# Optimization experiments

Hardware: AMD Instinct MI355X
Metric: run time of the kernel (lower is better)

The kernel has to match this reference:

```python
import jax, jax.numpy as jnp
import numpy as np

B, L, D = 4096, 200, 256
NUM_ITEMS, NUM_DT = 200000, 64


def setup_inputs() -> dict:
    key = jax.random.key(0)
    k1, k2, k3, k4, k5, k6 = jax.random.split(key, 6)
    items_pad = jax.random.randint(k1, (B, L), 0, NUM_ITEMS)
    dts_pad = jax.random.randint(k2, (B, L), 0, NUM_DT)
    mask = jnp.ones((B, L), dtype=bool)
    pos_items = jax.random.randint(k3, (B,), 0, NUM_ITEMS)
    neg_items = jax.random.randint(k4, (B,), 0, NUM_ITEMS)
    # embedding tables; row 0 zeroed to emulate padding_idx=0
    item_emb = jax.random.normal(k5, (NUM_ITEMS, D), dtype=jnp.float32).at[0].set(0.0)
    dt_gate = jax.random.normal(k6, (NUM_DT, 1), dtype=jnp.float32).at[0].set(0.0)
    raw_tau = jnp.float32(0.0)
    return {"items_pad": items_pad, "dts_pad": dts_pad, "mask": mask,
            "pos_items": pos_items, "neg_items": neg_items,
            "item_emb": item_emb, "dt_gate": dt_gate, "raw_tau": raw_tau}


def reference(items_pad, dts_pad, mask, pos_items, neg_items, item_emb, dt_gate, raw_tau):
    tau = jax.nn.softplus(raw_tau) + 1e-6
    k = item_emb[items_pad]                       # [B,L,D] history item embeddings
    gate = dt_gate[dts_pad, 0]                    # [B,L]  time-gate scalars

    def cand_aware_uservec(cand_items):
        q = item_emb[cand_items]                  # [B,D]
        sim = jnp.einsum('bld,bd->bl', k, q)      # candidate-aware similarity
        logits = jnp.where(mask, sim * gate / tau, -jnp.inf)
        attn = jax.nn.softmax(logits, axis=1)     # [B,L]
        u = jnp.einsum('bl,bld->bd', attn, k)     # weighted sum (bmm)
        return u, attn, q

    u_pos, attn_pos, q_pos = cand_aware_uservec(pos_items)
    u_neg, _, q_neg = cand_aware_uservec(neg_items)
    pos_score = jnp.sum(u_pos * q_pos, axis=-1)   # [B]
    neg_score = jnp.sum(u_neg * q_neg, axis=-1)   # [B]
    return pos_score, neg_score, attn_pos
```

## Files before the change

### kernel.cpp

```cpp
#include <hip/hip_runtime.h>
#include <math.h>

#define B_ 4096
#define L_ 200
#define D_ 256

__device__ __forceinline__ void dot8(const float* __restrict__ kp,
                                     const float qp[8], const float qn[8],
                                     float& sp, float& sn) {
    const float4 k0 = *(const float4*)kp;
    const float4 k1 = *(const float4*)(kp + 4);
    float a = 0.f, c = 0.f;
    a = fmaf(k0.x, qp[0], a); c = fmaf(k0.x, qn[0], c);
    a = fmaf(k0.y, qp[1], a); c = fmaf(k0.y, qn[1], c);
    a = fmaf(k0.z, qp[2], a); c = fmaf(k0.z, qn[2], c);
    a = fmaf(k0.w, qp[3], a); c = fmaf(k0.w, qn[3], c);
    a = fmaf(k1.x, qp[4], a); c = fmaf(k1.x, qn[4], c);
    a = fmaf(k1.y, qp[5], a); c = fmaf(k1.y, qn[5], c);
    a = fmaf(k1.z, qp[6], a); c = fmaf(k1.z, qn[6], c);
    a = fmaf(k1.w, qp[7], a); c = fmaf(k1.w, qn[7], c);
    sp = a; sn = c;
}

__global__ __launch_bounds__(256) void sic_f32(
    const int* __restrict__ items, const int* __restrict__ dts,
    const int* __restrict__ pos_items, const int* __restrict__ neg_items,
    const float* __restrict__ emb, const float* __restrict__ dt_gate,
    const float* __restrict__ raw_tau, float* __restrict__ out)
{
    const int b    = blockIdx.x;
    const int tid  = threadIdx.x;
    const int lane = tid & 63;
    const int wave = tid >> 6;
    const int half = lane >> 5;
    const int hl   = lane & 31;

    __shared__ int   s_items[L_];
    __shared__ float s_gate[L_];
    __shared__ float s_simp[L_], s_simn[L_];
    __shared__ float s_red[16];

    if (tid < L_) {
        s_items[tid] = items[b * L_ + tid];
        s_gate[tid]  = dt_gate[dts[b * L_ + tid]];
    }

    float qp[8], qn[8];
    {
        const float* pq = emb + (size_t)pos_items[b] * D_ + (size_t)hl * 8;
        const float* nq = emb + (size_t)neg_items[b] * D_ + (size_t)hl * 8;
        const float4 a0 = *(const float4*)pq, a1 = *(const float4*)(pq + 4);
        const float4 c0 = *(const float4*)nq, c1 = *(const float4*)(nq + 4);
        qp[0]=a0.x; qp[1]=a0.y; qp[2]=a0.z; qp[3]=a0.w;
        qp[4]=a1.x; qp[5]=a1.y; qp[6]=a1.z; qp[7]=a1.w;
        qn[0]=c0.x; qn[1]=c0.y; qn[2]=c0.z; qn[3]=c0.w;
        qn[4]=c1.x; qn[5]=c1.y; qn[6]=c1.z; qn[7]=c1.w;
    }
    __syncthreads();

    const int base = wave * 50;
#pragma unroll 2
    for (int t = 0; t < 12; ++t) {
        const int r0 = base + 4 * t + 2 * half;
        const float* k0p = emb + (size_t)s_items[r0]     * D_ + (size_t)hl * 8;
        const float* k1p = emb + (size_t)s_items[r0 + 1] * D_ + (size_t)hl * 8;
        float sp0, sn0, sp1, sn1;
        dot8(k0p, qp, qn, sp0, sn0);
        dot8(k1p, qp, qn, sp1, sn1);
#pragma unroll
        for (int off = 16; off; off >>= 1) {
            sp0 += __shfl_xor(sp0, off, 64);
            sn0 += __shfl_xor(sn0, off, 64);
            sp1 += __shfl_xor(sp1, off, 64);
            sn1 += __shfl_xor(sn1, off, 64);
        }
        if (hl == 0) {
            s_simp[r0]     = sp0; s_simn[r0]     = sn0;
            s_simp[r0 + 1] = sp1; s_simn[r0 + 1] = sn1;
        }
    }
    {
        const int r = base + 48 + half;
        const float* kp = emb + (size_t)s_items[r] * D_ + (size_t)hl * 8;
        float sp, sn;
        dot8(kp, qp, qn, sp, sn);
#pragma unroll
        for (int off = 16; off; off >>= 1) {
            sp += __shfl_xor(sp, off, 64);
            sn += __shfl_xor(sn, off, 64);
        }
        if (hl == 0) { s_simp[r] = sp; s_simn[r] = sn; }
    }
    __syncthreads();

    const float rt      = raw_tau[0];
    const float tau     = log1pf(expf(rt)) + 1e-6f;
    const float inv_tau = 1.0f / tau;

    float sp = 0.f, sn = 0.f, lp = -INFINITY, ln_ = -INFINITY;
    if (tid < L_) {
        sp = s_simp[tid]; sn = s_simn[tid];
        const float g = s_gate[tid] * inv_tau;
        lp  = sp * g;
        ln_ = sn * g;
    }

    float mp = lp, mn = ln_;
#pragma unroll
    for (int off = 32; off; off >>= 1) {
        mp = fmaxf(mp, __shfl_xor(mp, off, 64));
        mn = fmaxf(mn, __shfl_xor(mn, off, 64));
    }
    if (lane == 0) { s_red[wave] = mp; s_red[4 + wave] = mn; }
    __syncthreads();
    mp = fmaxf(fmaxf(s_red[0], s_red[1]), fmaxf(s_red[2], s_red[3]));
    mn = fmaxf(fmaxf(s_red[4], s_red[5]), fmaxf(s_red[6], s_red[7]));
    __syncthreads();

    float ep = 0.f, en = 0.f;
    if (tid < L_) { ep = expf(lp - mp); en = expf(ln_ - mn); }
    float v0 = ep, v1 = en, v2 = ep * sp, v3 = en * sn;
#pragma unroll
    for (int off = 32; off; off >>= 1) {
        v0 += __shfl_xor(v0, off, 64);
        v1 += __shfl_xor(v1, off, 64);
        v2 += __shfl_xor(v2, off, 64);
        v3 += __shfl_xor(v3, off, 64);
    }
    if (lane == 0) {
        s_red[wave]      = v0; s_red[4 + wave]  = v1;
        s_red[8 + wave]  = v2; s_red[12 + wave] = v3;
    }
    __syncthreads();
    const float sum_ep  = s_red[0]  + s_red[1]  + s_red[2]  + s_red[3];
    const float sum_en  = s_red[4]  + s_red[5]  + s_red[6]  + s_red[7];
    const float sum_eps = s_red[8]  + s_red[9]  + s_red[10] + s_red[11];
    const float sum_ens = s_red[12] + s_red[13] + s_red[14] + s_red[15];

    if (tid < L_) out[2 * B_ + (size_t)b * L_ + tid] = ep / sum_ep;
    if (tid == 0) {
        out[b]      = sum_eps / sum_ep;
        out[B_ + b] = sum_ens / sum_en;
    }
}

extern "C" void kernel_launch(void* const* d_in, const int* in_sizes, int n_in,
                              void* d_out, int out_size, void* d_ws, size_t ws_size,
                              hipStream_t stream) {
    const int* items     = (const int*)d_in[0];
    const int* dts       = (const int*)d_in[1];
    const int* pos_items = (const int*)d_in[3];
    const int* neg_items = (const int*)d_in[4];
    const float* item_emb = (const float*)d_in[5];
    const float* dt_gate  = (const float*)d_in[6];
    const float* raw_tau  = (const float*)d_in[7];
    float* out = (float*)d_out;

    sic_f32<<<B_, 256, 0, stream>>>(items, dts, pos_items, neg_items,
                                    item_emb, dt_gate, raw_tau, out);
}
```

Baseline: 361.4 us.

## Map one thread per history row with query vectors staged in LDS

Each thread now computes both candidate dot products for one full history row, instead of half a wavefront splitting a row and combining partials with shuffles. The positive and negative query embeddings are staged in shared memory, and the intermediate similarity and gate arrays in LDS disappear along with one barrier. The aim is to remove the cross-lane shuffle reductions and the shared-memory round trip. In exchange, lanes in a wavefront read different 1 KB rows, so global loads are no longer coalesced, 56 of 256 threads sit idle, and each thread runs a long serial FMA chain.

```diff
diff --git a/kernel.cpp b/kernel.cpp
--- a/kernel.cpp
+++ b/kernel.cpp
@@ -5,24 +5,7 @@
 #define L_ 200
 #define D_ 256
 
-__device__ __forceinline__ void dot8(const float* __restrict__ kp,
-                                     const float qp[8], const float qn[8],
-                                     float& sp, float& sn) {
-    const float4 k0 = *(const float4*)kp;
-    const float4 k1 = *(const float4*)(kp + 4);
-    float a = 0.f, c = 0.f;
-    a = fmaf(k0.x, qp[0], a); c = fmaf(k0.x, qn[0], c);
-    a = fmaf(k0.y, qp[1], a); c = fmaf(k0.y, qn[1], c);
-    a = fmaf(k0.z, qp[2], a); c = fmaf(k0.z, qn[2], c);
-    a = fmaf(k0.w, qp[3], a); c = fmaf(k0.w, qn[3], c);
-    a = fmaf(k1.x, qp[4], a); c = fmaf(k1.x, qn[4], c);
-    a = fmaf(k1.y, qp[5], a); c = fmaf(k1.y, qn[5], c);
-    a = fmaf(k1.z, qp[6], a); c = fmaf(k1.z, qn[6], c);
-    a = fmaf(k1.w, qp[7], a); c = fmaf(k1.w, qn[7], c);
-    sp = a; sn = c;
-}
-
-__global__ __launch_bounds__(256) void sic_f32(
+__global__ __launch_bounds__(256) void sic_tpr(
     const int* __restrict__ items, const int* __restrict__ dts,
     const int* __restrict__ pos_items, const int* __restrict__ neg_items,
     const float* __restrict__ emb, const float* __restrict__ dt_gate,
@@ -32,77 +15,43 @@
     const int tid  = threadIdx.x;
     const int lane = tid & 63;
     const int wave = tid >> 6;
-    const int half = lane >> 5;
-    const int hl   = lane & 31;
 
-    __shared__ int   s_items[L_];
-    __shared__ float s_gate[L_];
-    __shared__ float s_simp[L_], s_simn[L_];
-    __shared__ float s_red[16];
+    __shared__ float4 s_qp[D_ / 4];
+    __shared__ float4 s_qn[D_ / 4];
+    __shared__ float  s_red[16];
 
-    if (tid < L_) {
-        s_items[tid] = items[b * L_ + tid];
-        s_gate[tid]  = dt_gate[dts[b * L_ + tid]];
-    }
-
-    float qp[8], qn[8];
-    {
-        const float* pq = emb + (size_t)pos_items[b] * D_ + (size_t)hl * 8;
-        const float* nq = emb + (size_t)neg_items[b] * D_ + (size_t)hl * 8;
-        const float4 a0 = *(const float4*)pq, a1 = *(const float4*)(pq + 4);
-        const float4 c0 = *(const float4*)nq, c1 = *(const float4*)(nq + 4);
-        qp[0]=a0.x; qp[1]=a0.y; qp[2]=a0.z; qp[3]=a0.w;
-        qp[4]=a1.x; qp[5]=a1.y; qp[6]=a1.z; qp[7]=a1.w;
-        qn[0]=c0.x; qn[1]=c0.y; qn[2]=c0.z; qn[3]=c0.w;
-        qn[4]=c1.x; qn[5]=c1.y; qn[6]=c1.z; qn[7]=c1.w;
+    if (tid < 64) {
+        s_qp[tid] = ((const float4*)(emb + (size_t)pos_items[b] * D_))[tid];
+    } else if (tid < 128) {
+        s_qn[tid - 64] = ((const float4*)(emb + (size_t)neg_items[b] * D_))[tid - 64];
     }
     __syncthreads();
 
-    const int base = wave * 50;
-#pragma unroll 2
-    for (int t = 0; t < 12; ++t) {
-        const int r0 = base + 4 * t + 2 * half;
-        const float* k0p = emb + (size_t)s_items[r0]     * D_ + (size_t)hl * 8;
-        const float* k1p = emb + (size_t)s_items[r0 + 1] * D_ + (size_t)hl * 8;
-        float sp0, sn0, sp1, sn1;
-        dot8(k0p, qp, qn, sp0, sn0);
-        dot8(k1p, qp, qn, sp1, sn1);
-#pragma unroll
-        for (int off = 16; off; off >>= 1) {
-            sp0 += __shfl_xor(sp0, off, 64);
-            sn0 += __shfl_xor(sn0, off, 64);
-            sp1 += __shfl_xor(sp1, off, 64);
-            sn1 += __shfl_xor(sn1, off, 64);
-        }
-        if (hl == 0) {
-            s_simp[r0]     = sp0; s_simn[r0]     = sn0;
-            s_simp[r0 + 1] = sp1; s_simn[r0 + 1] = sn1;
+    float sp = 0.f, sn = 0.f, g = 0.f;
+    if (tid < L_) {
+        const int row = items[b * L_ + tid];
+        g = dt_gate[dts[b * L_ + tid]];
+        const float4* kr = (const float4*)(emb + (size_t)row * D_);
+#pragma unroll 8
+        for (int j = 0; j < D_ / 4; ++j) {
+            const float4 kv = kr[j];
+            const float4 qp = s_qp[j];
+            const float4 qn = s_qn[j];
+            sp = fmaf(kv.x, qp.x, sp); sn = fmaf(kv.x, qn.x, sn);
+            sp = fmaf(kv.y, qp.y, sp); sn = fmaf(kv.y, qn.y, sn);
+            sp = fmaf(kv.z, qp.z, sp); sn = fmaf(kv.z, qn.z, sn);
+            sp = fmaf(kv.w, qp.w, sp); sn = fmaf(kv.w, qn.w, sn);
         }
     }
-    {
-        const int r = base + 48 + half;
-        const float* kp = emb + (size_t)s_items[r] * D_ + (size_t)hl * 8;
-        float sp, sn;
-        dot8(kp, qp, qn, sp, sn);
-#pragma unroll
-        for (int off = 16; off; off >>= 1) {
-            sp += __shfl_xor(sp, off, 64);
-            sn += __shfl_xor(sn, off, 64);
-        }
-        if (hl == 0) { s_simp[r] = sp; s_simn[r] = sn; }
-    }
-    __syncthreads();
 
-    const float rt      = raw_tau[0];
-    const float tau     = log1pf(expf(rt)) + 1e-6f;
+    const float tau     = log1pf(expf(raw_tau[0])) + 1e-6f;
     const float inv_tau = 1.0f / tau;
 
-    float sp = 0.f, sn = 0.f, lp = -INFINITY, ln_ = -INFINITY;
+    float lp = -INFINITY, ln_ = -INFINITY;
     if (tid < L_) {
-        sp = s_simp[tid]; sn = s_simn[tid];
-        const float g = s_gate[tid] * inv_tau;
-        lp  = sp * g;
-        ln_ = sn * g;
+        const float gs = g * inv_tau;
+        lp  = sp * gs;
+        ln_ = sn * gs;
     }
 
     float mp = lp, mn = ln_;
@@ -156,6 +105,6 @@
     const float* raw_tau  = (const float*)d_in[7];
     float* out = (float*)d_out;
 
-    sic_f32<<<B_, 256, 0, stream>>>(items, dts, pos_items, neg_items,
+    sic_tpr<<<B_, 256, 0, stream>>>(items, dts, pos_items, neg_items,
                                     item_emb, dt_gate, raw_tau, out);
 }
```

After: 407.1 us. 1.13x slower.
